# Kernel tuning notes

Measured on AMD Instinct MI355X. Metric: run time of the kernel, lower is better.

The kernel has to match this reference:

```python
import jax, jax.numpy as jnp
import numpy as np

B = 8192
E = 8
H = 128
NUM_CLASSES = 3
SIM_THRESHOLD = 0.8
EFF_THRESHOLD = 0.1
TARGET_TEMP = 1.0
W_LB, W_EFF, W_CONS, W_ENT, W_TEMP = 0.1, 0.05, 0.1, 0.01, 0.01


def setup_inputs() -> dict:
    key = jax.random.key(0)
    k1, k2, k3, k4 = jax.random.split(key, 4)
    logits = jax.random.normal(k1, (B, NUM_CLASSES), dtype=jnp.float32)
    targets = jax.random.randint(k2, (B,), 0, NUM_CLASSES, dtype=jnp.int64)
    raw = jax.random.uniform(k3, (B, E), dtype=jnp.float32)
    routing_probs = raw / raw.sum(axis=-1, keepdims=True)  # rows sum to 1
    input_embeddings = jax.random.uniform(k4, (B, H), dtype=jnp.float32)
    temperature = jnp.ones((1,), dtype=jnp.float32)
    return {
        "logits": logits,
        "targets": targets,
        "routing_probs": routing_probs,
        "input_embeddings": input_embeddings,
        "temperature": temperature,
    }


def _dynamo_loss(logits, routing_probs, input_embeddings, temperature, targets):
    # --- task loss: cross entropy (sentiment) ---
    logp_cls = jax.nn.log_softmax(logits, axis=-1)
    task_loss = -jnp.take_along_axis(logp_cls, targets[:, None], axis=-1).mean()

    # --- load balance: var(mean usage) / (1/E)^2 (torch.var unbiased) ---
    expert_usage = routing_probs.mean(axis=0)  # [E]
    lb_loss = W_LB * jnp.var(expert_usage, ddof=1) * (E ** 2)

    # --- efficiency: sum of probs below threshold, averaged over batch ---
    small = jnp.where(routing_probs < EFF_THRESHOLD, routing_probs, 0.0)
    eff_loss = W_EFF * small.sum(axis=-1).mean()

    # --- consistency: masked pairwise KL over similar samples ---
    nrm = input_embeddings / jnp.linalg.norm(input_embeddings, axis=-1, keepdims=True)
    sim = nrm @ nrm.T  # [B, B]
    mask = (sim > SIM_THRESHOLD) & ~jnp.eye(B, dtype=bool)
    logp = jax.nn.log_softmax(routing_probs, axis=-1)  # [B, E]
    p = jnp.exp(logp)
    a = jnp.sum(p * logp, axis=-1)  # [B], sum_e p_j log p_j
    # KL(i,j) = sum_e p_j (log p_j - log p_i) = a[j] - logp[i] . p[j]
    kl = a[None, :] - logp @ p.T  # [B, B]
    num_pairs = mask.sum()
    kl_sum = jnp.sum(jnp.where(mask, kl, 0.0))
    cons_loss = W_CONS * jnp.where(num_pairs > 0, kl_sum / jnp.maximum(num_pairs, 1), 0.0)

    # --- entropy regularization (maximize entropy of routing_probs-as-probs) ---
    eps = 1e-8
    entropy = -jnp.sum(routing_probs * jnp.log(routing_probs + eps), axis=-1)
    ent_loss = W_ENT * (-entropy.mean())

    # --- temperature regularization ---
    temp_loss = W_TEMP * jnp.mean((temperature - TARGET_TEMP) ** 2)

    return task_loss + lb_loss + eff_loss + cons_loss + ent_loss + temp_loss


def reference(logits, targets, routing_probs, input_embeddings, temperature):
    return _dynamo_loss(logits, routing_probs, input_embeddings, temperature, targets)
```

## Files before the change

### kernel.cpp

```cpp
#include <hip/hip_runtime.h>
#include <stdint.h>

#define B_SZ 8192
#define LOG8 2.0794415416798357f
#define NTILE 4160

typedef __attribute__((ext_vector_type(8))) short short8;
typedef __attribute__((ext_vector_type(4))) float floatx4;

typedef __attribute__((address_space(1))) const uint4 guint4;
typedef __attribute__((address_space(3))) uint4 luint4;

__device__ inline void async_cp16(const uint4* g, uint4* l) {
    __builtin_amdgcn_global_load_lds((guint4*)g, (luint4*)l, 16, 0, 0);
}

__device__ inline unsigned short f2bf(float f) {
    unsigned int u = __float_as_uint(f);
    u = (u + 0x7FFFu + ((u >> 16) & 1u)) >> 16;
    return (unsigned short)u;
}
__device__ inline float bf2f(unsigned short s) {
    return __uint_as_float(((unsigned int)s) << 16);
}
__device__ inline float wredf(float x) {
#pragma unroll
    for (int o = 32; o; o >>= 1) x += __shfl_down(x, o);
    return x;
}
__device__ inline int wredi(int x) {
#pragma unroll
    for (int o = 32; o; o >>= 1) x += __shfl_down(x, o);
    return x;
}


__global__ __launch_bounds__(512) void prep_all(
    const float* __restrict__ logits,
    const int* __restrict__ targets,
    const float* __restrict__ routing,
    const float* __restrict__ emb,
    unsigned short* __restrict__ nrm,
    unsigned short* __restrict__ nlq,
    unsigned short* __restrict__ pb,
    float* __restrict__ aprime,
    float* __restrict__ prepslot) {
    __shared__ float pred[8][11];
    const int bid = blockIdx.x;
    const int lane = threadIdx.x & 63;
    const int wave = threadIdx.x >> 6;

    if (bid < 256) {
#pragma unroll
        for (int iter = 0; iter < 4; ++iter) {
            int row = (((iter << 8) + bid) << 3) + wave;
            const float2* e2 = (const float2*)(emb + (size_t)row * 128);
            float2 v = e2[lane];
            float ss = v.x * v.x + v.y * v.y;
            ss = wredf(ss);
            ss = __shfl(ss, 0);
            float inv = rsqrtf(ss);
            ushort2 o;
            o.x = f2bf(v.x * inv);
            o.y = f2bf(v.y * inv);
            ((ushort2*)(nrm + (size_t)row * 128))[lane] = o;
        }
        return;
    }

    int row = ((bid - 256) << 9) + threadIdx.x;

    const float4* r4 = (const float4*)(routing + (size_t)row * 8);
    float4 va = r4[0], vb = r4[1];
    float v[8] = {va.x, va.y, va.z, va.w, vb.x, vb.y, vb.z, vb.w};

    float mx = v[0];
#pragma unroll
    for (int e = 1; e < 8; ++e) mx = fmaxf(mx, v[e]);
    float ex[8], s = 0.f;
#pragma unroll
    for (int e = 0; e < 8; ++e) { ex[e] = expf(v[e] - mx); s += ex[e]; }
    float ls = logf(s);
    float inv_s = 1.f / s;

    union { unsigned short u[8]; uint4 q; } lu, pu;
    float ap = 0.f;
#pragma unroll
    for (int e = 0; e < 8; ++e) {
        unsigned short pe = f2bf(ex[e] * inv_s);
        unsigned short le = f2bf(v[e] - mx - ls + LOG8);
        pu.u[e] = pe;
        lu.u[e] = le ^ 0x8000;
        ap += bf2f(pe) * bf2f(le);
    }
    ((uint4*)nlq)[row] = lu.q;
    ((uint4*)pb)[row] = pu.q;
    aprime[row] = ap;

    float eff = 0.f, ent = 0.f;
#pragma unroll
    for (int e = 0; e < 8; ++e) {
        if (v[e] < 0.1f) eff += v[e];
        ent += v[e] * logf(v[e] + 1e-8f);
    }

    const float* lg = logits + (size_t)row * 3;
    float a0 = lg[0], a1 = lg[1], a2 = lg[2];
    float mm = fmaxf(a0, fmaxf(a1, a2));
    float lse = mm + logf(expf(a0 - mm) + expf(a1 - mm) + expf(a2 - mm));
    int tg = targets[row];
    float tv = (tg == 0) ? a0 : ((tg == 1) ? a1 : a2);
    float task = lse - tv;

    task = wredf(task);
    eff = wredf(eff);
    ent = wredf(ent);
    float cs[8];
#pragma unroll
    for (int e = 0; e < 8; ++e) cs[e] = wredf(v[e]);

    if (lane == 0) {
        pred[wave][0] = task;
        pred[wave][1] = eff;
        pred[wave][2] = ent;
#pragma unroll
        for (int e = 0; e < 8; ++e) pred[wave][3 + e] = cs[e];
    }
    __syncthreads();
    if (threadIdx.x < 11) {
        float s2 = 0.f;
#pragma unroll
        for (int w = 0; w < 8; ++w) s2 += pred[w][threadIdx.x];
        prepslot[(bid - 256) * 11 + threadIdx.x] = s2;
    }
}

__global__ __launch_bounds__(512, 4) void tile_sym(
    const unsigned short* __restrict__ nrm,
    const unsigned short* __restrict__ nlq,
    const unsigned short* __restrict__ pb,
    const float* __restrict__ aprime,
    float* __restrict__ klslot,
    unsigned int* __restrict__ cntslot) {
    __shared__ uint4 sh[3072];

    const int t = threadIdx.x;
    const int L = blockIdx.x;
    const int wave = t >> 6, lane = t & 63;

    int bi = (int)((129.0f - sqrtf((float)(16641 - 4 * L))) * 0.5f);
    int T = bi * (129 - bi);
    while (L < T) { --bi; T = bi * (129 - bi); }
    while (L >= T + (128 - 2 * bi)) { T += 128 - 2 * bi; ++bi; }
    const int bj = 2 * bi + (L - T);
    const bool strip = ((bj >> 1) == bi);
    const int iBase = bi << 7, jBase = bj << 6;

    const uint4* n4 = (const uint4*)nrm;

#pragma unroll
    for (int it = 0; it < 4; ++it) {
        int idx = t + (it << 9);
        int row = idx >> 4, s = idx & 15;
        int g = s ^ (row & 15);
        async_cp16(&n4[((size_t)(iBase + row) << 4) + g],
                   sh + (it << 9) + (wave << 6));
    }
#pragma unroll
    for (int it = 0; it < 2; ++it) {
        int idx = t + (it << 9);
        int row = idx >> 4, s = idx & 15;
        int g = s ^ (row & 15);
        async_cp16(&n4[((size_t)(jBase + row) << 4) + g],
                   sh + 2048 + (it << 9) + (wave << 6));
    }

    const int wr = wave >> 2, wc = wave & 3;
    const int m = lane & 15, q = lane >> 4;
    const short8 zero8 = (short8){0, 0, 0, 0, 0, 0, 0, 0};

    short8 crA[4], crB;
#pragma unroll
    for (int a = 0; a < 4; ++a) {
        int ri = iBase + (wr << 6) + (a << 4) + m;
        short8 v = zero8;
        if (q == 0) v = *(const short8*)&nlq[(size_t)ri << 3];
        else if (q == 1) { if (!strip) v = *(const short8*)&pb[(size_t)ri << 3]; }
        else if (q == 2) {
            v[1] = (short)0x3F80;
            if (!strip) v[0] = (short)f2bf(aprime[ri]);
        }
        crA[a] = v;
    }
    {
        int cj = jBase + (wc << 4) + m;
        short8 v = zero8;
        if (q == 0) v = *(const short8*)&pb[(size_t)cj << 3];
        else if (q == 1) v = *(const short8*)&nlq[(size_t)cj << 3];
        else if (q == 2) {
            v[0] = (short)0x3F80;
            v[1] = (short)f2bf(aprime[cj]);
        }
        crB = v;
    }

    __syncthreads();

    floatx4 simacc[4];
#pragma unroll
    for (int a = 0; a < 4; ++a) simacc[a] = (floatx4){0.f, 0.f, 0.f, 0.f};

#pragma unroll
    for (int ks = 0; ks < 4; ++ks) {
        const int gk = (ks << 2) + q;
        short8 bfr;
        {
            int rb = (wc << 4) + m;
            bfr = *(const short8*)(sh + 2048 + (rb << 4) + (gk ^ m));
        }
        short8 af[4];
#pragma unroll
        for (int a = 0; a < 4; ++a) {
            int row = (wr << 6) + (a << 4) + m;
            af[a] = *(const short8*)(sh + (row << 4) + (gk ^ m));
        }
#pragma unroll
        for (int a = 0; a < 4; ++a)
            simacc[a] = __builtin_amdgcn_mfma_f32_16x16x32_bf16(
                af[a], bfr, simacc[a], 0, 0, 0);
    }

    float klLocal = 0.f;
    int cntLocal = 0;
    const int gCol = jBase + (wc << 4) + m;
#pragma unroll
    for (int a = 0; a < 4; ++a) {
        const int gRow0 = iBase + (wr << 6) + (a << 4) + (q << 2);
        floatx4 cr = __builtin_amdgcn_mfma_f32_16x16x32_bf16(
            crA[a], crB, (floatx4){0.f, 0.f, 0.f, 0.f}, 0, 0, 0);
        if (strip) {
#pragma unroll
            for (int r = 0; r < 4; ++r) {
                if ((simacc[a][r] > 0.8f) && (gRow0 + r != gCol)) {
                    klLocal += cr[r];
                    cntLocal += 1;
                }
            }
        } else {
#pragma unroll
            for (int r = 0; r < 4; ++r) {
                if (simacc[a][r] > 0.8f) {
                    klLocal += cr[r];
                    cntLocal += 2;
                }
            }
        }
    }

    klLocal = wredf(klLocal);
    cntLocal = wredi(cntLocal);

    __syncthreads();
    float* redk = (float*)sh;
    int* redc = (int*)(redk + 8);
    if (lane == 0) { redk[wave] = klLocal; redc[wave] = cntLocal; }
    __syncthreads();

    if (t == 0) {
        float k = 0.f;
        int c = 0;
#pragma unroll
        for (int w = 0; w < 8; ++w) { k += redk[w]; c += redc[w]; }
        klslot[L] = k;
        cntslot[L] = (unsigned int)c;
    }
}

__global__ void finalize_k(const float* __restrict__ klslot,
                           const unsigned int* __restrict__ cntslot,
                           const float* __restrict__ prepslot,
                           const float* __restrict__ temp,
                           float* __restrict__ out) {
    __shared__ float sk[4];
    __shared__ int sc[4];
    __shared__ float sp[11];
    const int t = threadIdx.x, lane = t & 63, wave = t >> 6;

    float k = 0.f;
    int c = 0;
    for (int i = t; i < NTILE; i += 256) { k += klslot[i]; c += (int)cntslot[i]; }
    k = wredf(k);
    c = wredi(c);
    if (lane == 0) { sk[wave] = k; sc[wave] = c; }
    if (t < 11) {
        float s = 0.f;
        for (int r = 0; r < 16; ++r) s += prepslot[r * 11 + t];
        sp[t] = s;
    }
    __syncthreads();
    if (t == 0) {
        float K = sk[0] + sk[1] + sk[2] + sk[3];
        int C = sc[0] + sc[1] + sc[2] + sc[3];
        const float invB = 1.f / (float)B_SZ;
        float task = sp[0] * invB;
        float eff = 0.05f * sp[1] * invB;
        float entl = 0.01f * sp[2] * invB;
        float cons = 0.1f * (C > 0 ? K / (float)C : 0.f);
        float u[8], mean = 0.f;
        for (int e = 0; e < 8; ++e) { u[e] = sp[3 + e] * invB; mean += u[e]; }
        mean *= 0.125f;
        float var = 0.f;
        for (int e = 0; e < 8; ++e) { float d = u[e] - mean; var += d * d; }
        var *= (1.f / 7.f);
        float lb = 0.1f * var * 64.f;
        float tt = temp[0] - 1.f;
        out[0] = task + lb + eff + cons + entl + 0.01f * tt * tt;
    }
}

extern "C" void kernel_launch(void* const* d_in, const int* in_sizes, int n_in,
                              void* d_out, int out_size, void* d_ws, size_t ws_size,
                              hipStream_t stream) {
    const float* logits = (const float*)d_in[0];
    const int* targets = (const int*)d_in[1];
    const float* routing = (const float*)d_in[2];
    const float* emb = (const float*)d_in[3];
    const float* temp = (const float*)d_in[4];

    char* ws = (char*)d_ws;
    unsigned short* nrm = (unsigned short*)ws;
    unsigned short* nlq = (unsigned short*)(ws + 2097152);
    unsigned short* pb = (unsigned short*)(ws + 2228224);
    float* aprime = (float*)(ws + 2359296);
    float* klslot = (float*)(ws + 2392064);
    unsigned int* cntslot = (unsigned int*)(ws + 2408704);
    float* prepslot = (float*)(ws + 2425344);

    prep_all<<<272, 512, 0, stream>>>(logits, targets, routing, emb,
                                      nrm, nlq, pb, aprime, prepslot);
    tile_sym<<<NTILE, 512, 0, stream>>>(nrm, nlq, pb, aprime, klslot, cntslot);
    finalize_k<<<1, 256, 0, stream>>>(klslot, cntslot, prepslot, temp,
                                      (float*)d_out);
}
```

Baseline: 109.9 us.

## Process up to eight column tiles per block with double-buffered LDS loads

Each block now keeps its 128-row A panel resident in LDS and loops over up to eight 64-column B tiles. The next B tile is prefetched asynchronously into a second buffer while the current one is computed. This cuts the grid from 4160 to 544 blocks and removes repeated A-panel loads and per-block setup and reduction overhead. The cost is a sequential loop with a barrier per tile, more LDS per block, and fewer blocks to spread across the CUs, which can leave the tail unbalanced.

```diff
diff --git a/kernel.cpp b/kernel.cpp
--- a/kernel.cpp
+++ b/kernel.cpp
@@ -3,7 +3,7 @@
 
 #define B_SZ 8192
 #define LOG8 2.0794415416798357f
-#define NTILE 4160
+#define NCHUNK 544
 
 typedef __attribute__((ext_vector_type(8))) short short8;
 typedef __attribute__((ext_vector_type(4))) float floatx4;
@@ -142,19 +142,22 @@
     const float* __restrict__ aprime,
     float* __restrict__ klslot,
     unsigned int* __restrict__ cntslot) {
-    __shared__ uint4 sh[3072];
+    __shared__ uint4 sh[4096];
 
     const int t = threadIdx.x;
-    const int L = blockIdx.x;
     const int wave = t >> 6, lane = t & 63;
 
-    int bi = (int)((129.0f - sqrtf((float)(16641 - 4 * L))) * 0.5f);
-    int T = bi * (129 - bi);
-    while (L < T) { --bi; T = bi * (129 - bi); }
-    while (L >= T + (128 - 2 * bi)) { T += 128 - 2 * bi; ++bi; }
-    const int bj = 2 * bi + (L - T);
-    const bool strip = ((bj >> 1) == bi);
-    const int iBase = bi << 7, jBase = bj << 6;
+    int bi = 0, rem = blockIdx.x;
+    for (;;) {
+        int nc = (135 - 2 * bi) >> 3;
+        if (rem < nc) break;
+        rem -= nc;
+        ++bi;
+    }
+    const int c = rem;
+    const int bj0 = 2 * bi + (c << 3);
+    const int nt = min(8, 128 - bj0);
+    const int iBase = bi << 7;
 
     const uint4* n4 = (const uint4*)nrm;
 
@@ -166,101 +169,133 @@
         async_cp16(&n4[((size_t)(iBase + row) << 4) + g],
                    sh + (it << 9) + (wave << 6));
     }
-#pragma unroll
-    for (int it = 0; it < 2; ++it) {
-        int idx = t + (it << 9);
-        int row = idx >> 4, s = idx & 15;
-        int g = s ^ (row & 15);
-        async_cp16(&n4[((size_t)(jBase + row) << 4) + g],
-                   sh + 2048 + (it << 9) + (wave << 6));
+    {
+        const int jB = bj0 << 6;
+#pragma unroll
+        for (int it = 0; it < 2; ++it) {
+            int idx = t + (it << 9);
+            int row = idx >> 4, s = idx & 15;
+            int g = s ^ (row & 15);
+            async_cp16(&n4[((size_t)(jB + row) << 4) + g],
+                       sh + 2048 + (it << 9) + (wave << 6));
+        }
     }
 
     const int wr = wave >> 2, wc = wave & 3;
     const int m = lane & 15, q = lane >> 4;
     const short8 zero8 = (short8){0, 0, 0, 0, 0, 0, 0, 0};
 
-    short8 crA[4], crB;
+    short8 crA[4];
 #pragma unroll
     for (int a = 0; a < 4; ++a) {
         int ri = iBase + (wr << 6) + (a << 4) + m;
         short8 v = zero8;
         if (q == 0) v = *(const short8*)&nlq[(size_t)ri << 3];
-        else if (q == 1) { if (!strip) v = *(const short8*)&pb[(size_t)ri << 3]; }
+        else if (q == 1) v = *(const short8*)&pb[(size_t)ri << 3];
         else if (q == 2) {
+            v[0] = (short)f2bf(aprime[ri]);
             v[1] = (short)0x3F80;
-            if (!strip) v[0] = (short)f2bf(aprime[ri]);
         }
         crA[a] = v;
     }
-    {
-        int cj = jBase + (wc << 4) + m;
-        short8 v = zero8;
-        if (q == 0) v = *(const short8*)&pb[(size_t)cj << 3];
-        else if (q == 1) v = *(const short8*)&nlq[(size_t)cj << 3];
-        else if (q == 2) {
-            v[0] = (short)0x3F80;
-            v[1] = (short)f2bf(aprime[cj]);
-        }
-        crB = v;
-    }
 
     __syncthreads();
-
-    floatx4 simacc[4];
-#pragma unroll
-    for (int a = 0; a < 4; ++a) simacc[a] = (floatx4){0.f, 0.f, 0.f, 0.f};
-
-#pragma unroll
-    for (int ks = 0; ks < 4; ++ks) {
-        const int gk = (ks << 2) + q;
-        short8 bfr;
-        {
-            int rb = (wc << 4) + m;
-            bfr = *(const short8*)(sh + 2048 + (rb << 4) + (gk ^ m));
-        }
-        short8 af[4];
-#pragma unroll
-        for (int a = 0; a < 4; ++a) {
-            int row = (wr << 6) + (a << 4) + m;
-            af[a] = *(const short8*)(sh + (row << 4) + (gk ^ m));
-        }
-#pragma unroll
-        for (int a = 0; a < 4; ++a)
-            simacc[a] = __builtin_amdgcn_mfma_f32_16x16x32_bf16(
-                af[a], bfr, simacc[a], 0, 0, 0);
-    }
 
     float klLocal = 0.f;
     int cntLocal = 0;
-    const int gCol = jBase + (wc << 4) + m;
-#pragma unroll
-    for (int a = 0; a < 4; ++a) {
-        const int gRow0 = iBase + (wr << 6) + (a << 4) + (q << 2);
-        floatx4 cr = __builtin_amdgcn_mfma_f32_16x16x32_bf16(
-            crA[a], crB, (floatx4){0.f, 0.f, 0.f, 0.f}, 0, 0, 0);
-        if (strip) {
-#pragma unroll
-            for (int r = 0; r < 4; ++r) {
-                if ((simacc[a][r] > 0.8f) && (gRow0 + r != gCol)) {
-                    klLocal += cr[r];
-                    cntLocal += 1;
+
+#pragma unroll 1
+    for (int tt = 0; tt < nt; ++tt) {
+        const int bj = bj0 + tt;
+        const int jBase = bj << 6;
+        const bool strip = ((bj >> 1) == bi);
+        const int cur = 2048 + ((tt & 1) << 10);
+
+        if (tt + 1 < nt) {
+            const int jN = (bj + 1) << 6;
+            const int nxt = 2048 + (((tt + 1) & 1) << 10);
+#pragma unroll
+            for (int it = 0; it < 2; ++it) {
+                int idx = t + (it << 9);
+                int row = idx >> 4, s = idx & 15;
+                int g = s ^ (row & 15);
+                async_cp16(&n4[((size_t)(jN + row) << 4) + g],
+                           sh + nxt + (it << 9) + (wave << 6));
+            }
+        }
+
+        short8 crB;
+        {
+            int cj = jBase + (wc << 4) + m;
+            short8 v = zero8;
+            if (q == 0) v = *(const short8*)&pb[(size_t)cj << 3];
+            else if (q == 1) v = *(const short8*)&nlq[(size_t)cj << 3];
+            else if (q == 2) {
+                v[0] = (short)0x3F80;
+                v[1] = (short)f2bf(aprime[cj]);
+            }
+            crB = v;
+        }
+
+        floatx4 simacc[4];
+#pragma unroll
+        for (int a = 0; a < 4; ++a) simacc[a] = (floatx4){0.f, 0.f, 0.f, 0.f};
+#pragma unroll
+        for (int ks = 0; ks < 4; ++ks) {
+            const int gk = (ks << 2) + q;
+            short8 bfr;
+            {
+                int rb = (wc << 4) + m;
+                bfr = *(const short8*)(sh + cur + (rb << 4) + (gk ^ m));
+            }
+            short8 af[4];
+#pragma unroll
+            for (int a = 0; a < 4; ++a) {
+                int row = (wr << 6) + (a << 4) + m;
+                af[a] = *(const short8*)(sh + (row << 4) + (gk ^ m));
+            }
+#pragma unroll
+            for (int a = 0; a < 4; ++a)
+                simacc[a] = __builtin_amdgcn_mfma_f32_16x16x32_bf16(
+                    af[a], bfr, simacc[a], 0, 0, 0);
+        }
+
+        const int gCol = jBase + (wc << 4) + m;
+#pragma unroll
+        for (int a = 0; a < 4; ++a) {
+            short8 ca = crA[a];
+            if (strip) {
+                if (q == 1) ca = zero8;
+                else if (q == 2) ca[0] = 0;
+            }
+            floatx4 cr = __builtin_amdgcn_mfma_f32_16x16x32_bf16(
+                ca, crB, (floatx4){0.f, 0.f, 0.f, 0.f}, 0, 0, 0);
+            const int gRow0 = iBase + (wr << 6) + (a << 4) + (q << 2);
+            if (strip) {
+#pragma unroll
+                for (int r = 0; r < 4; ++r) {
+                    if ((simacc[a][r] > 0.8f) && (gRow0 + r != gCol)) {
+                        klLocal += cr[r];
+                        cntLocal += 1;
+                    }
                 }
-            }
-        } else {
-#pragma unroll
-            for (int r = 0; r < 4; ++r) {
-                if (simacc[a][r] > 0.8f) {
-                    klLocal += cr[r];
-                    cntLocal += 2;
+            } else {
+#pragma unroll
+                for (int r = 0; r < 4; ++r) {
+                    if (simacc[a][r] > 0.8f) {
+                        klLocal += cr[r];
+                        cntLocal += 2;
+                    }
                 }
             }
         }
+
+        __syncthreads();
     }
 
     klLocal = wredf(klLocal);
     cntLocal = wredi(cntLocal);
 
-    __syncthreads();
     float* redk = (float*)sh;
     int* redc = (int*)(redk + 8);
     if (lane == 0) { redk[wave] = klLocal; redc[wave] = cntLocal; }
@@ -268,11 +303,11 @@
 
     if (t == 0) {
         float k = 0.f;
-        int c = 0;
-#pragma unroll
-        for (int w = 0; w < 8; ++w) { k += redk[w]; c += redc[w]; }
-        klslot[L] = k;
-        cntslot[L] = (unsigned int)c;
+        int cc = 0;
+#pragma unroll
+        for (int w = 0; w < 8; ++w) { k += redk[w]; cc += redc[w]; }
+        klslot[blockIdx.x] = k;
+        cntslot[blockIdx.x] = (unsigned int)cc;
     }
 }
 
@@ -288,7 +323,7 @@
 
     float k = 0.f;
     int c = 0;
-    for (int i = t; i < NTILE; i += 256) { k += klslot[i]; c += (int)cntslot[i]; }
+    for (int i = t; i < NCHUNK; i += 256) { k += klslot[i]; c += (int)cntslot[i]; }
     k = wredf(k);
     c = wredi(c);
     if (lane == 0) { sk[wave] = k; sc[wave] = c; }
@@ -333,12 +368,12 @@
     unsigned short* pb = (unsigned short*)(ws + 2228224);
     float* aprime = (float*)(ws + 2359296);
     float* klslot = (float*)(ws + 2392064);
-    unsigned int* cntslot = (unsigned int*)(ws + 2408704);
-    float* prepslot = (float*)(ws + 2425344);
+    unsigned int* cntslot = (unsigned int*)(ws + 2394304);
+    float* prepslot = (float*)(ws + 2396544);
 
     prep_all<<<272, 512, 0, stream>>>(logits, targets, routing, emb,
                                       nrm, nlq, pb, aprime, prepslot);
-    tile_sym<<<NTILE, 512, 0, stream>>>(nrm, nlq, pb, aprime, klslot, cntslot);
+    tile_sym<<<NCHUNK, 512, 0, stream>>>(nrm, nlq, pb, aprime, klslot, cntslot);
     finalize_k<<<1, 256, 0, stream>>>(klslot, cntslot, prepslot, temp,
                                       (float*)d_out);
 }
```

Measured after the change: 105.9 us. -3.7%, faster.
